# Optimization experiments

Measured on AMD Instinct MI355X. Metric: run time of the kernel, lower is better.

## Reference

```python
import jax, jax.numpy as jnp
import numpy as np

B, S, D, H = 128, 256, 256, 8
EPS = 1e-5

def ln(x, g, b):
    m = x.mean(-1, keepdims=True)
    v = x.var(-1, keepdims=True)
    return (x - m) / jnp.sqrt(v + EPS) * g + b

def setup_inputs() -> dict:
    key = jax.random.key(0)
    ks = jax.random.split(key, 16)
    w = lambda k, sh: (jax.random.normal(k, sh, dtype=jnp.float32) * 0.02)
    HD = H * D
    return {
        "local": jax.random.normal(ks[0], (B, D), dtype=jnp.float32),
        "dist": jax.random.normal(ks[1], (B, S, D), dtype=jnp.float32),
        "sites": jax.random.normal(ks[2], (B, S, D), dtype=jnp.float32),
        "mask": jax.random.randint(ks[3], (B, 1, S), 0, 2).astype(bool),
        "Wq": w(ks[4], (D, HD)), "bq": jnp.zeros((HD,), jnp.float32),
        "gq": jnp.ones((HD,), jnp.float32), "betq": jnp.zeros((HD,), jnp.float32),
        "Wk": w(ks[5], (D, HD)), "bk": jnp.zeros((HD,), jnp.float32),
        "gk": jnp.ones((HD,), jnp.float32), "betk": jnp.zeros((HD,), jnp.float32),
        "Wv": w(ks[6], (D, HD)), "bv": jnp.zeros((HD,), jnp.float32),
        "gv": jnp.ones((HD,), jnp.float32), "betv": jnp.zeros((HD,), jnp.float32),
        "g1": jnp.ones((HD,), jnp.float32), "b1": jnp.zeros((HD,), jnp.float32),
        "Wo": w(ks[7], (HD, D)), "bo": jnp.zeros((D,), jnp.float32),
        "g2": jnp.ones((D,), jnp.float32), "b2": jnp.zeros((D,), jnp.float32),
        "Wa": w(ks[8], (H, 1)), "ba": jnp.zeros((1,), jnp.float32),
        "ga": jnp.ones((1,), jnp.float32), "beta_a": jnp.zeros((1,), jnp.float32),
    }

def reference(local, dist, sites, mask, Wq, bq, gq, betq, Wk, bk, gk, betk,
              Wv, bv, gv, betv, g1, b1, Wo, bo, g2, b2, Wa, ba, ga, beta_a):
    # QKV projections + LayerNorm over H*D
    q = ln(local @ Wq + bq, gq, betq)            # [B, H*D]
    k = ln(dist @ Wk + bk, gk, betk)             # [B, S, H*D]
    v = ln(sites @ Wv + bv, gv, betv)            # [B, S, H*D]
    # split heads, layout [H, B, q/s, D] matching torch permute(2,0,1,3)
    q4 = q.reshape(B, 1, H, D).transpose(2, 0, 1, 3)   # [H,B,1,D]
    k4 = k.reshape(B, S, H, D).transpose(2, 0, 1, 3)   # [H,B,S,D]
    v4 = v.reshape(B, S, H, D).transpose(2, 0, 1, 3)   # [H,B,S,D]
    u = jnp.einsum('hbqd,hbsd->hbqs', q4, k4) / jnp.sqrt(jnp.float32(S))
    u = jnp.where(mask[None], -jnp.inf, u)             # mask [B,1,S] broadcasts over heads
    attn = jax.nn.softmax(u, axis=-1)                  # [H,B,1,S]
    out = jnp.einsum('hbqs,hbsd->hbqd', attn, v4) + q4 # residual add, [H,B,1,D]
    out = out.transpose(1, 2, 0, 3).reshape(B, 1, H * D)
    out = ln(ln(out, g1, b1) @ Wo + bo, g2, b2)        # [B,1,D]
    # faithful raw view: [B,1,H,S] contiguous reinterpreted as [B,S,H]
    attn_r = attn.transpose(1, 2, 0, 3).reshape(B, S, H)
    a = ln(attn_r @ Wa + ba, ga, beta_a)               # [B,S,1]
    a = jnp.swapaxes(a, -1, -2)                        # [B,1,S]
    return (a, out)
```

## Files before the change

### kernel.cpp

```cpp
#include <hip/hip_runtime.h>

#define NB 128
#define NS 256
#define ND 256
#define NH 8
#define NHD 2048
static constexpr float EPS = 1e-5f;

typedef __attribute__((ext_vector_type(8))) short bf8v;
typedef __attribute__((ext_vector_type(4))) float f32x4;

__device__ __forceinline__ short f2bf(float f) {
  unsigned u = __float_as_uint(f);
  unsigned r = (u + 0x7fffu + ((u >> 16) & 1u)) >> 16;
  return (short)r;
}

__device__ __forceinline__ void split8(float4 a, float4 b, bf8v& hi, bf8v& lo) {
  float x[8] = {a.x, a.y, a.z, a.w, b.x, b.y, b.z, b.w};
  bf8v h, l;
#pragma unroll
  for (int i = 0; i < 8; ++i) {
    unsigned u = __float_as_uint(x[i]);
    unsigned hb = (u + 0x7fffu + ((u >> 16) & 1u)) >> 16;
    h[i] = (short)hb;
    float hf = __uint_as_float(hb << 16);
    l[i] = f2bf(x[i] - hf);
  }
  hi = h;
  lo = l;
}

__device__ __forceinline__ float block_reduce_sum(float v, float* red, int t) {
  __syncthreads();
  red[t] = v;
  __syncthreads();
  for (int off = 128; off > 0; off >>= 1) {
    if (t < off) red[t] += red[t + off];
    __syncthreads();
  }
  return red[0];
}

__global__ __launch_bounds__(256) void k_meta(const float* __restrict__ Wk,
                                              const float* __restrict__ bk,
                                              const float* __restrict__ Wv,
                                              const float* __restrict__ bv,
                                              const int* __restrict__ mask_i,
                                              float* __restrict__ kmeta,
                                              float* __restrict__ vmeta,
                                              int* __restrict__ flag) {
  int sel = blockIdx.y, c = blockIdx.x, t = threadIdx.x;
  const float* W = sel ? Wv : Wk;
  const float* bvec = sel ? bv : bk;
  float* meta = sel ? vmeta : kmeta;
  __shared__ float red[256];
  __shared__ int sflag;
  float s_w = 0.f, s_l = 0.f;
  const float* row = W + (size_t)c * NHD;
  for (int j = t; j < NHD; j += 256) { float w = row[j]; s_w += w; s_l += w * bvec[j]; }
  s_w = block_reduce_sum(s_w, red, t);
  s_l = block_reduce_sum(s_l, red, t);
  if (t == 0) { meta[c] = s_w * (1.0f / NHD); meta[256 + c] = s_l * (2.0f / NHD); }
  if (c == 0) {
    float s_b = 0.f, s_b2 = 0.f;
    for (int j = t; j < NHD; j += 256) { float bb = bvec[j]; s_b += bb; s_b2 += bb * bb; }
    s_b = block_reduce_sum(s_b, red, t);
    s_b2 = block_reduce_sum(s_b2, red, t);
    if (t == 0) { meta[512] = s_b * (1.0f / NHD); meta[513] = s_b2 * (1.0f / NHD); }
  }
  if (c == 1 && sel == 0) {
    if (t == 0) sflag = 0;
    __syncthreads();
    int any = 0;
    for (int i = t; i < 8192; i += 256) {
      unsigned v = (unsigned)mask_i[i];
      if (v > 1u) any = 1;
    }
    if (any) atomicOr(&sflag, 1);
    __syncthreads();
    if (t == 0) flag[0] = sflag;
  }
}

__global__ __launch_bounds__(256) void k_aat2(const float* __restrict__ Wk,
                                              const float* __restrict__ Wv,
                                              float* __restrict__ MkP,
                                              float* __restrict__ MvP) {
  int idx = blockIdx.x, bi = 0;
  while (idx >= 8 - bi) { idx -= 8 - bi; ++bi; }
  int bj = bi + idx;
  int sel = blockIdx.y & 1, kchunk = blockIdx.y >> 1;
  const float* A = sel ? Wv : Wk;
  float* outP = (sel ? MvP : MkP) + kchunk * 65536;
  int t = threadIdx.x;
  int w = t >> 6, l = t & 63, r16 = l & 15, ksub = l >> 4;
  __shared__ float red[4][32][33];

  int k0 = kchunk * 512 + w * 128;
  const float* ar0 = A + (size_t)(bi * 32 + r16) * NHD + k0;
  const float* ar1 = ar0 + 16 * NHD;
  const float* br0 = A + (size_t)(bj * 32 + r16) * NHD + k0;
  const float* br1 = br0 + 16 * NHD;

  bf8v ah[2][4], al[2][4], bh[2][4], bl[2][4];
#pragma unroll
  for (int kk = 0; kk < 4; ++kk) {
    int c0 = kk * 32 + ksub * 8;
    split8(*(const float4*)(ar0 + c0), *(const float4*)(ar0 + c0 + 4), ah[0][kk], al[0][kk]);
    split8(*(const float4*)(ar1 + c0), *(const float4*)(ar1 + c0 + 4), ah[1][kk], al[1][kk]);
    split8(*(const float4*)(br0 + c0), *(const float4*)(br0 + c0 + 4), bh[0][kk], bl[0][kk]);
    split8(*(const float4*)(br1 + c0), *(const float4*)(br1 + c0 + 4), bh[1][kk], bl[1][kk]);
  }
  f32x4 acc[2][2];
#pragma unroll
  for (int gi = 0; gi < 2; ++gi)
#pragma unroll
    for (int gj = 0; gj < 2; ++gj) acc[gi][gj] = (f32x4){0.f, 0.f, 0.f, 0.f};
#pragma unroll
  for (int kk = 0; kk < 4; ++kk) {
#pragma unroll
    for (int gi = 0; gi < 2; ++gi)
#pragma unroll
      for (int gj = 0; gj < 2; ++gj) {
        acc[gi][gj] = __builtin_amdgcn_mfma_f32_16x16x32_bf16(ah[gi][kk], bh[gj][kk], acc[gi][gj], 0, 0, 0);
        acc[gi][gj] = __builtin_amdgcn_mfma_f32_16x16x32_bf16(al[gi][kk], bh[gj][kk], acc[gi][gj], 0, 0, 0);
        acc[gi][gj] = __builtin_amdgcn_mfma_f32_16x16x32_bf16(ah[gi][kk], bl[gj][kk], acc[gi][gj], 0, 0, 0);
      }
  }
#pragma unroll
  for (int gi = 0; gi < 2; ++gi)
#pragma unroll
    for (int gj = 0; gj < 2; ++gj)
#pragma unroll
      for (int q = 0; q < 4; ++q)
        red[w][gi * 16 + ksub * 4 + q][gj * 16 + r16] = acc[gi][gj][q];
  __syncthreads();
  int r = t >> 3, c0 = (t & 7) * 4;
#pragma unroll
  for (int c = c0; c < c0 + 4; ++c) {
    float s = (red[0][r][c] + red[1][r][c]) + (red[2][r][c] + red[3][r][c]);
    outP[(size_t)(bi * 32 + r) * 256 + bj * 32 + c] = s;
  }
  if (bi != bj) {
#pragma unroll
    for (int c = c0; c < c0 + 4; ++c) {
      float s = (red[0][c][r] + red[1][c][r]) + (red[2][c][r] + red[3][c][r]);
      outP[(size_t)(bj * 32 + r) * 256 + bi * 32 + c] = s;
    }
  }
}

__global__ __launch_bounds__(256) void k_aat_reduce(const float* __restrict__ MkP,
                                                    const float* __restrict__ MvP,
                                                    short* __restrict__ Mkb,
                                                    short* __restrict__ Mvb) {
  int sel = blockIdx.y;
  const float* P = sel ? MvP : MkP;
  short* O = sel ? Mvb : Mkb;
  int idx = blockIdx.x * 256 + threadIdx.x;
  float s = (P[idx] + P[65536 + idx] + P[131072 + idx] + P[196608 + idx]) * (1.0f / NHD);
  O[idx] = f2bf(s);
}

__global__ __launch_bounds__(256) void k_q1(const float* __restrict__ local,
                                            const float* __restrict__ Wq,
                                            const float* __restrict__ bq,
                                            float* __restrict__ qraw,
                                            float* __restrict__ qpart) {
  int h = blockIdx.x, b = blockIdx.y, t = threadIdx.x;
  __shared__ float ls[256];
  __shared__ float red[256];
  ls[t] = local[b * ND + t];
  __syncthreads();
  int j = h * 256 + t;
  float a0 = 0.f, a1 = 0.f, a2 = 0.f, a3 = 0.f;
  const float* W = Wq + j;
#pragma unroll 4
  for (int c = 0; c < 256; c += 4) {
    a0 = fmaf(ls[c],     W[(size_t)c * NHD], a0);
    a1 = fmaf(ls[c + 1], W[(size_t)(c + 1) * NHD], a1);
    a2 = fmaf(ls[c + 2], W[(size_t)(c + 2) * NHD], a2);
    a3 = fmaf(ls[c + 3], W[(size_t)(c + 3) * NHD], a3);
  }
  float acc = (a0 + a1) + (a2 + a3) + bq[j];
  qraw[(size_t)b * NHD + j] = acc;
  float s1 = block_reduce_sum(acc, red, t);
  float s2 = block_reduce_sum(acc * acc, red, t);
  if (t == 0) { qpart[(b * 8 + h) * 2] = s1; qpart[(b * 8 + h) * 2 + 1] = s2; }
}

__global__ __launch_bounds__(256) void k_wkeff(const float* __restrict__ qraw,
                                               const float* __restrict__ qpart,
                                               const float* __restrict__ gq,
                                               const float* __restrict__ betq,
                                               const float* __restrict__ Wk,
                                               const float* __restrict__ bk,
                                               const float* __restrict__ gk,
                                               const float* __restrict__ betk,
                                               float* __restrict__ wkeff,
                                               float* __restrict__ cbGT) {
  int h = blockIdx.x, b = blockIdx.y, t = threadIdx.x;
  __shared__ float qg[256];
  __shared__ float red[256];
  float s1 = 0.f, s2 = 0.f;
#pragma unroll
  for (int i = 0; i < 8; ++i) { s1 += qpart[(b * 8 + i) * 2]; s2 += qpart[(b * 8 + i) * 2 + 1]; }
  float m = s1 * (1.0f / NHD);
  float var = s2 * (1.0f / NHD) - m * m;
  float is = 1.0f / sqrtf(var + EPS);
  int j = h * 256 + t;
  float q = (qraw[(size_t)b * NHD + j] - m) * is * gq[j] + betq[j];
  float qgv = q * gk[j];
  qg[t] = qgv;
  float cb = block_reduce_sum(bk[j] * qgv, red, t);
  float G = block_reduce_sum(qgv, red, t);
  float T = block_reduce_sum(q * betk[j], red, t);
  float acc = 0.f;
  const float4* wr = (const float4*)(Wk + (size_t)t * NHD + h * 256);
#pragma unroll 4
  for (int d4 = 0; d4 < 64; ++d4) {
    float4 w = wr[d4];
    acc += w.x * qg[d4 * 4] + w.y * qg[d4 * 4 + 1] + w.z * qg[d4 * 4 + 2] + w.w * qg[d4 * 4 + 3];
  }
  wkeff[(size_t)(b * NH + h) * ND + t] = acc;
  if (t == 0) { float* p = cbGT + (b * NH + h) * 4; p[0] = cb; p[1] = G; p[2] = T; }
}

__global__ __launch_bounds__(256) void k_moments(const float* __restrict__ dist,
                                                 const float* __restrict__ sites,
                                                 const short* __restrict__ Mkb,
                                                 const short* __restrict__ Mvb,
                                                 const float* __restrict__ kmeta,
                                                 const float* __restrict__ vmeta,
                                                 float* __restrict__ mk_arr,
                                                 float* __restrict__ sk_arr,
                                                 float* __restrict__ mv_arr,
                                                 float* __restrict__ sv_arr) {
  int sel = blockIdx.y;
  const float* X = sel ? sites : dist;
  const short* Mb = sel ? Mvb : Mkb;
  const float* meta = sel ? vmeta : kmeta;
  float* m_out = sel ? mv_arr : mk_arr;
  float* s_out = sel ? sv_arr : sk_arr;

  int t = threadIdx.x;
  int w = t >> 6;
  int l = t & 63;
  int r16 = l & 15;
  int ksub = l >> 4;
  int srow = t >> 4;
  int scc0 = (t & 15) * 8;

  __shared__ __align__(16) short Tb[4][2][16][40];
  __shared__ __align__(16) short Ms[2][16][264];

  for (int cc = scc0; cc < 32; cc += 128)
    *(bf8v*)&Ms[0][srow][cc] = *(const bf8v*)(Mb + ((size_t)srow << 8) + cc);

  size_t rowA = (size_t)blockIdx.x * 128 + w * 32;
  const float* xr0 = X + (rowA + r16) * 256;
  const float* xr1 = xr0 + 16 * 256;

  bf8v af0[8], af1[8];
  float pm0 = 0.f, pl0 = 0.f, pm1 = 0.f, pl1 = 0.f;
#pragma unroll
  for (int kc = 0; kc < 8; ++kc) {
    int c0 = kc * 32 + ksub * 8;
    float4 wa = *(const float4*)(meta + c0);
    float4 wb = *(const float4*)(meta + c0 + 4);
    float4 la = *(const float4*)(meta + 256 + c0);
    float4 lb = *(const float4*)(meta + 256 + c0 + 4);
    float4 x0a = *(const float4*)(xr0 + c0);
    float4 x0b = *(const float4*)(xr0 + c0 + 4);
    float4 x1a = *(const float4*)(xr1 + c0);
    float4 x1b = *(const float4*)(xr1 + c0 + 4);
    pm0 += x0a.x * wa.x + x0a.y * wa.y + x0a.z * wa.z + x0a.w * wa.w
         + x0b.x * wb.x + x0b.y * wb.y + x0b.z * wb.z + x0b.w * wb.w;
    pl0 += x0a.x * la.x + x0a.y * la.y + x0a.z * la.z + x0a.w * la.w
         + x0b.x * lb.x + x0b.y * lb.y + x0b.z * lb.z + x0b.w * lb.w;
    pm1 += x1a.x * wa.x + x1a.y * wa.y + x1a.z * wa.z + x1a.w * wa.w
         + x1b.x * wb.x + x1b.y * wb.y + x1b.z * wb.z + x1b.w * wb.w;
    pl1 += x1a.x * la.x + x1a.y * la.y + x1a.z * la.z + x1a.w * la.w
         + x1b.x * lb.x + x1b.y * lb.y + x1b.z * lb.z + x1b.w * lb.w;
    bf8v a0, a1;
    a0[0] = f2bf(x0a.x); a0[1] = f2bf(x0a.y); a0[2] = f2bf(x0a.z); a0[3] = f2bf(x0a.w);
    a0[4] = f2bf(x0b.x); a0[5] = f2bf(x0b.y); a0[6] = f2bf(x0b.z); a0[7] = f2bf(x0b.w);
    a1[0] = f2bf(x1a.x); a1[1] = f2bf(x1a.y); a1[2] = f2bf(x1a.z); a1[3] = f2bf(x1a.w);
    a1[4] = f2bf(x1b.x); a1[5] = f2bf(x1b.y); a1[6] = f2bf(x1b.z); a1[7] = f2bf(x1b.w);
    af0[kc] = a0;
    af1[kc] = a1;
  }
  pm0 += __shfl_xor(pm0, 16); pm0 += __shfl_xor(pm0, 32);
  pl0 += __shfl_xor(pl0, 16); pl0 += __shfl_xor(pl0, 32);
  pm1 += __shfl_xor(pm1, 16); pm1 += __shfl_xor(pm1, 32);
  pl1 += __shfl_xor(pl1, 16); pl1 += __shfl_xor(pl1, 32);

  __syncthreads();

  f32x4 y0 = {0.f, 0.f, 0.f, 0.f}, y1 = {0.f, 0.f, 0.f, 0.f};

#pragma unroll
  for (int n = 0; n < 16; ++n) {
    if (n < 15) {
      const int nn = n + 1;
      const int ncols = 32 * ((nn >> 1) + 1);
      for (int cc = scc0; cc < ncols; cc += 128)
        *(bf8v*)&Ms[nn & 1][srow][cc] = *(const bf8v*)(Mb + ((size_t)(nn * 16 + srow) << 8) + cc);
    }
    const int kcd = n >> 1;
    f32x4 ta = {0.f, 0.f, 0.f, 0.f}, tb = {0.f, 0.f, 0.f, 0.f};
#pragma unroll
    for (int kc = 0; kc < kcd; ++kc) {
      bf8v bfv = *(const bf8v*)&Ms[n & 1][r16][kc * 32 + ksub * 8];
      ta = __builtin_amdgcn_mfma_f32_16x16x32_bf16(af0[kc], bfv, ta, 0, 0, 0);
      tb = __builtin_amdgcn_mfma_f32_16x16x32_bf16(af1[kc], bfv, tb, 0, 0, 0);
    }
    ta = ta + ta;
    tb = tb + tb;
    {
      bf8v bfd = *(const bf8v*)&Ms[n & 1][r16][kcd * 32 + ksub * 8];
      ta = __builtin_amdgcn_mfma_f32_16x16x32_bf16(af0[kcd], bfd, ta, 0, 0, 0);
      tb = __builtin_amdgcn_mfma_f32_16x16x32_bf16(af1[kcd], bfd, tb, 0, 0, 0);
    }
#pragma unroll
    for (int q = 0; q < 4; ++q) {
      Tb[w][0][ksub * 4 + q][(n & 1) * 16 + r16] = f2bf(ta[q]);
      Tb[w][1][ksub * 4 + q][(n & 1) * 16 + r16] = f2bf(tb[q]);
    }
    if (n & 1) {
      bf8v a20 = *(const bf8v*)&Tb[w][0][r16][ksub * 8];
      bf8v a21 = *(const bf8v*)&Tb[w][1][r16][ksub * 8];
      y0 = __builtin_amdgcn_mfma_f32_16x16x32_bf16(a20, af0[n >> 1], y0, 0, 0, 0);
      y1 = __builtin_amdgcn_mfma_f32_16x16x32_bf16(a21, af1[n >> 1], y1, 0, 0, 0);
    }
    __syncthreads();
  }

  int qs = r16 & 3;
  float yd0 = (qs == 0) ? y0[0] : (qs == 1) ? y0[1] : (qs == 2) ? y0[2] : y0[3];
  float yd1 = (qs == 0) ? y1[0] : (qs == 1) ? y1[1] : (qs == 2) ? y1[2] : y1[3];
  float bbar = meta[512], cc = meta[513];
  if (ksub == (r16 >> 2)) {
    float m0 = pm0 + bbar;
    float var0 = fmaxf(yd0 + (pl0 + cc) - m0 * m0, 0.0f) + EPS;
    m_out[rowA + r16] = m0;
    s_out[rowA + r16] = 1.0f / sqrtf(var0);
    float m1 = pm1 + bbar;
    float var1 = fmaxf(yd1 + (pl1 + cc) - m1 * m1, 0.0f) + EPS;
    m_out[rowA + 16 + r16] = m1;
    s_out[rowA + 16 + r16] = 1.0f / sqrtf(var1);
  }
}

__global__ __launch_bounds__(512) void k_attn2(const float* __restrict__ dist,
                                               const float* __restrict__ sites,
                                               const int* __restrict__ mask_i,
                                               const int* __restrict__ mflag,
                                               const float* __restrict__ wkeff,
                                               const float* __restrict__ cbGT,
                                               const float* __restrict__ mk_arr,
                                               const float* __restrict__ sk_arr,
                                               const float* __restrict__ mv_arr,
                                               const float* __restrict__ sv_arr,
                                               float* __restrict__ zbuf,
                                               float* __restrict__ bg) {
  int b = blockIdx.x, t = threadIdx.x;
  int w = t >> 6, l = t & 63, r16 = l & 15, ksub = l >> 4;

  __shared__ float us[16][260];
  __shared__ __align__(16) short St[256][72];

  for (int i = t; i < 8 * 260; i += 512) (&us[8][0])[i] = 0.f;

  const int mbytes = mflag[0];

  const float* xr0 = dist + ((size_t)b * NS + w * 32 + r16) * ND;
  const float* xr1 = xr0 + 16 * ND;
  const float* wkp = wkeff + ((size_t)b * NH + (r16 & 7)) * ND;
  f32x4 u0 = {0.f, 0.f, 0.f, 0.f}, u1 = {0.f, 0.f, 0.f, 0.f};
#pragma unroll 2
  for (int kc = 0; kc < 8; ++kc) {
    int c0 = kc * 32 + ksub * 8;
    float4 xa = *(const float4*)(xr0 + c0);
    float4 xb = *(const float4*)(xr0 + c0 + 4);
    float4 ya = *(const float4*)(xr1 + c0);
    float4 yb = *(const float4*)(xr1 + c0 + 4);
    float4 wa = {0.f, 0.f, 0.f, 0.f}, wb = {0.f, 0.f, 0.f, 0.f};
    if (r16 < 8) { wa = *(const float4*)(wkp + c0); wb = *(const float4*)(wkp + c0 + 4); }
    bf8v xh, xl, yh, yl, wh, wl;
    split8(xa, xb, xh, xl);
    split8(ya, yb, yh, yl);
    split8(wa, wb, wh, wl);
    u0 = __builtin_amdgcn_mfma_f32_16x16x32_bf16(xh, wh, u0, 0, 0, 0);
    u0 = __builtin_amdgcn_mfma_f32_16x16x32_bf16(xl, wh, u0, 0, 0, 0);
    u0 = __builtin_amdgcn_mfma_f32_16x16x32_bf16(xh, wl, u0, 0, 0, 0);
    u1 = __builtin_amdgcn_mfma_f32_16x16x32_bf16(yh, wh, u1, 0, 0, 0);
    u1 = __builtin_amdgcn_mfma_f32_16x16x32_bf16(yl, wh, u1, 0, 0, 0);
    u1 = __builtin_amdgcn_mfma_f32_16x16x32_bf16(yh, wl, u1, 0, 0, 0);
  }

  float cb = 0.f, G = 0.f, T = 0.f;
  if (r16 < 8) { const float* p = cbGT + (b * NH + r16) * 4; cb = p[0]; G = p[1]; T = p[2]; }
  const unsigned char* mask_b = (const unsigned char*)mask_i;
#pragma unroll
  for (int g = 0; g < 2; ++g) {
    f32x4 uu = g ? u1 : u0;
    int base = w * 32 + g * 16 + ksub * 4;
    float4 mk4 = *(const float4*)(mk_arr + b * NS + base);
    float4 sk4 = *(const float4*)(sk_arr + b * NS + base);
    int mm[4];
    if (mbytes) {
      mm[0] = mask_b[b * NS + base];     mm[1] = mask_b[b * NS + base + 1];
      mm[2] = mask_b[b * NS + base + 2]; mm[3] = mask_b[b * NS + base + 3];
    } else {
      mm[0] = mask_i[b * NS + base];     mm[1] = mask_i[b * NS + base + 1];
      mm[2] = mask_i[b * NS + base + 2]; mm[3] = mask_i[b * NS + base + 3];
    }
    const float* mkp = (const float*)&mk4;
    const float* skp = (const float*)&sk4;
#pragma unroll
    for (int q = 0; q < 4; ++q) {
      float u = ((uu[q] + cb - mkp[q] * G) * skp[q] + T) * 0.0625f;
      if (mm[q]) u = -1e30f;
      if (r16 < 8) us[r16][base + q] = u;
    }
  }
  __syncthreads();

  {
    int h = w;
    float v[4];
#pragma unroll
    for (int i = 0; i < 4; ++i) v[i] = us[h][l + 64 * i];
    float mx = fmaxf(fmaxf(v[0], v[1]), fmaxf(v[2], v[3]));
    for (int off = 32; off > 0; off >>= 1) mx = fmaxf(mx, __shfl_xor(mx, off));
    float sum = 0.f;
#pragma unroll
    for (int i = 0; i < 4; ++i) { v[i] = expf(v[i] - mx); sum += v[i]; }
    for (int off = 32; off > 0; off >>= 1) sum += __shfl_xor(sum, off);
    float inv = 1.0f / sum;
    float bp = 0.f, gp = 0.f;
#pragma unroll
    for (int i = 0; i < 4; ++i) {
      int s = l + 64 * i;
      float a = v[i] * inv;
      float sv = sv_arr[b * NS + s];
      float mv = mv_arr[b * NS + s];
      float wv = a * sv;
      us[h][s] = wv;
      bp += wv;
      gp += wv * mv;
    }
    for (int off = 32; off > 0; off >>= 1) { bp += __shfl_xor(bp, off); gp += __shfl_xor(gp, off); }
    if (l == 0) { float* p = bg + (b * NH + h) * 2; p[0] = bp; p[1] = gp; }
  }
  __syncthreads();

  f32x4 z0 = {0.f, 0.f, 0.f, 0.f}, z1 = {0.f, 0.f, 0.f, 0.f};
  int half = t >> 8, tc = t & 255;
  for (int chunk = 0; chunk < 4; ++chunk) {
    const float* Sp = sites + ((size_t)b * NS + chunk * 64) * ND + tc;
#pragma unroll
    for (int it = 0; it < 4; ++it) {
      int s8 = (half * 4 + it) * 8;
      bf8v vtmp;
#pragma unroll
      for (int j = 0; j < 8; ++j) vtmp[j] = f2bf(Sp[(size_t)(s8 + j) * ND]);
      *(bf8v*)&St[tc][s8] = vtmp;
    }
    __syncthreads();
#pragma unroll
    for (int kst = 0; kst < 2; ++kst) {
      int sg = chunk * 64 + kst * 32 + ksub * 8;
      int sl0 = kst * 32 + ksub * 8;
      float4 p0 = *(const float4*)&us[r16][sg];
      float4 p1 = *(const float4*)&us[r16][sg + 4];
      bf8v ah, al;
      split8(p0, p1, ah, al);
      bf8v b0 = *(const bf8v*)&St[(2 * w) * 16 + r16][sl0];
      bf8v b1 = *(const bf8v*)&St[(2 * w + 1) * 16 + r16][sl0];
      z0 = __builtin_amdgcn_mfma_f32_16x16x32_bf16(ah, b0, z0, 0, 0, 0);
      z0 = __builtin_amdgcn_mfma_f32_16x16x32_bf16(al, b0, z0, 0, 0, 0);
      z1 = __builtin_amdgcn_mfma_f32_16x16x32_bf16(ah, b1, z1, 0, 0, 0);
      z1 = __builtin_amdgcn_mfma_f32_16x16x32_bf16(al, b1, z1, 0, 0, 0);
    }
    __syncthreads();
  }
  if (ksub < 2) {
#pragma unroll
    for (int q = 0; q < 4; ++q) {
      int h = ksub * 4 + q;
      zbuf[((size_t)b * NH + h) * ND + 2 * w * 16 + r16] = z0[q];
      zbuf[((size_t)b * NH + h) * ND + (2 * w + 1) * 16 + r16] = z1[q];
    }
  }
}

__global__ __launch_bounds__(256) void k_o1(const float* __restrict__ zbuf,
                                            const float* __restrict__ bg,
                                            const float* __restrict__ qraw,
                                            const float* __restrict__ qpart,
                                            const float* __restrict__ gq,
                                            const float* __restrict__ betq,
                                            const float* __restrict__ Wv,
                                            const float* __restrict__ bv,
                                            const float* __restrict__ gv,
                                            const float* __restrict__ betv,
                                            float* __restrict__ o_buf,
                                            float* __restrict__ part1) {
  int h = blockIdx.x, b = blockIdx.y, t = threadIdx.x;
  __shared__ float zs[256];
  __shared__ float red[256];
  zs[t] = zbuf[((size_t)b * NH + h) * ND + t];
  __syncthreads();
  float qs1 = 0.f, qs2 = 0.f;
#pragma unroll
  for (int i = 0; i < 8; ++i) { qs1 += qpart[(b * 8 + i) * 2]; qs2 += qpart[(b * 8 + i) * 2 + 1]; }
  float qm = qs1 * (1.0f / NHD);
  float qvar = qs2 * (1.0f / NHD) - qm * qm;
  float qis = 1.0f / sqrtf(qvar + EPS);
  float bets = bg[(b * NH + h) * 2], gams = bg[(b * NH + h) * 2 + 1];
  int j = h * 256 + t;
  float a0 = 0.f, a1 = 0.f, a2 = 0.f, a3 = 0.f;
  const float* W = Wv + j;
#pragma unroll 4
  for (int c = 0; c < 256; c += 4) {
    a0 = fmaf(zs[c],     W[(size_t)c * NHD], a0);
    a1 = fmaf(zs[c + 1], W[(size_t)(c + 1) * NHD], a1);
    a2 = fmaf(zs[c + 2], W[(size_t)(c + 2) * NHD], a2);
    a3 = fmaf(zs[c + 3], W[(size_t)(c + 3) * NHD], a3);
  }
  float acc = (a0 + a1) + (a2 + a3);
  float qln = (qraw[(size_t)b * NHD + j] - qm) * qis * gq[j] + betq[j];
  float o = gv[j] * (acc + bv[j] * bets - gams) + betv[j] + qln;
  o_buf[(size_t)b * NHD + j] = o;
  float s1 = block_reduce_sum(o, red, t);
  float s2 = block_reduce_sum(o * o, red, t);
  if (t == 0) { part1[(b * 8 + h) * 2] = s1; part1[(b * 8 + h) * 2 + 1] = s2; }
}

__global__ __launch_bounds__(256) void k_o2(const float* __restrict__ o_buf,
                                            const float* __restrict__ part1,
                                            const float* __restrict__ g1,
                                            const float* __restrict__ b1,
                                            const float* __restrict__ Wo,
                                            float* __restrict__ part2) {
  int ks = blockIdx.x, b = blockIdx.y, t = threadIdx.x;
  __shared__ float y1s[256];
  float s1 = 0.f, s2 = 0.f;
#pragma unroll
  for (int i = 0; i < 8; ++i) { s1 += part1[(b * 8 + i) * 2]; s2 += part1[(b * 8 + i) * 2 + 1]; }
  float m = s1 * (1.0f / NHD);
  float var = s2 * (1.0f / NHD) - m * m;
  float is = 1.0f / sqrtf(var + EPS);
  int jj = ks * 256 + t;
  y1s[t] = (o_buf[(size_t)b * NHD + jj] - m) * is * g1[jj] + b1[jj];
  __syncthreads();
  float a0 = 0.f, a1 = 0.f, a2 = 0.f, a3 = 0.f;
  const float* W = Wo + (size_t)ks * 256 * 256 + t;
#pragma unroll 4
  for (int i = 0; i < 256; i += 4) {
    a0 = fmaf(y1s[i],     W[(size_t)i * 256], a0);
    a1 = fmaf(y1s[i + 1], W[(size_t)(i + 1) * 256], a1);
    a2 = fmaf(y1s[i + 2], W[(size_t)(i + 2) * 256], a2);
    a3 = fmaf(y1s[i + 3], W[(size_t)(i + 3) * 256], a3);
  }
  part2[((size_t)ks * NB + b) * 256 + t] = (a0 + a1) + (a2 + a3);
}

__global__ __launch_bounds__(256) void k_o3(const float* __restrict__ part2,
                                            const float* __restrict__ bo,
                                            const float* __restrict__ g2,
                                            const float* __restrict__ b2,
                                            const float* __restrict__ beta_a,
                                            float* __restrict__ out) {
  int b = blockIdx.x, t = threadIdx.x;
  __shared__ float red[256];
  float acc = bo[t];
#pragma unroll
  for (int ks = 0; ks < 8; ++ks) acc += part2[((size_t)ks * NB + b) * 256 + t];
  float q1 = block_reduce_sum(acc, red, t);
  float q2 = block_reduce_sum(acc * acc, red, t);
  float m2 = q1 * (1.0f / 256.0f);
  float v2 = q2 * (1.0f / 256.0f) - m2 * m2;
  float is2 = 1.0f / sqrtf(v2 + EPS);
  out[NB * NS + b * 256 + t] = (acc - m2) * is2 * g2[t] + b2[t];
  out[b * 256 + t] = beta_a[0];
}

extern "C" void kernel_launch(void* const* d_in, const int* in_sizes, int n_in,
                              void* d_out, int out_size, void* d_ws, size_t ws_size,
                              hipStream_t stream) {
  (void)in_sizes; (void)n_in; (void)out_size; (void)ws_size;
  const float* local = (const float*)d_in[0];
  const float* dist  = (const float*)d_in[1];
  const float* sites = (const float*)d_in[2];
  const int*   mask  = (const int*)d_in[3];
  const float* Wq   = (const float*)d_in[4];
  const float* bq   = (const float*)d_in[5];
  const float* gq   = (const float*)d_in[6];
  const float* betq = (const float*)d_in[7];
  const float* Wk   = (const float*)d_in[8];
  const float* bk   = (const float*)d_in[9];
  const float* gk   = (const float*)d_in[10];
  const float* betk = (const float*)d_in[11];
  const float* Wv   = (const float*)d_in[12];
  const float* bv   = (const float*)d_in[13];
  const float* gv   = (const float*)d_in[14];
  const float* betv = (const float*)d_in[15];
  const float* g1   = (const float*)d_in[16];
  const float* b1   = (const float*)d_in[17];
  const float* Wo   = (const float*)d_in[18];
  const float* bo   = (const float*)d_in[19];
  const float* g2   = (const float*)d_in[20];
  const float* b2   = (const float*)d_in[21];
  const float* beta_a = (const float*)d_in[25];
  float* out = (float*)d_out;

  float* ws = (float*)d_ws;
  float* MkP   = ws;
  float* MvP   = MkP + 262144;
  short* Mkb   = (short*)(MvP + 262144);
  short* Mvb   = Mkb + 65536;
  float* kmeta = (float*)(Mvb + 65536);
  float* vmeta = kmeta + 1024;
  float* qraw  = vmeta + 1024;
  float* wkeff = qraw + 262144;
  float* cbGT  = wkeff + 262144;
  float* mk_arr = cbGT + 4096;
  float* sk_arr = mk_arr + 32768;
  float* mv_arr = sk_arr + 32768;
  float* sv_arr = mv_arr + 32768;
  float* zbuf  = sv_arr + 32768;
  float* bg    = zbuf + 262144;
  int*   mflag = (int*)(bg + 2048);
  float* part1 = (float*)(mflag + 16);
  float* qpart = part1 + 2048;

  float* o_buf = qraw;
  float* part2 = MvP;

  k_meta<<<dim3(256, 2), dim3(256), 0, stream>>>(Wk, bk, Wv, bv, mask, kmeta, vmeta, mflag);
  k_aat2<<<dim3(36, 8), dim3(256), 0, stream>>>(Wk, Wv, MkP, MvP);
  k_aat_reduce<<<dim3(256, 2), dim3(256), 0, stream>>>(MkP, MvP, Mkb, Mvb);
  k_q1<<<dim3(8, 128), dim3(256), 0, stream>>>(local, Wq, bq, qraw, qpart);
  k_wkeff<<<dim3(8, 128), dim3(256), 0, stream>>>(qraw, qpart, gq, betq, Wk, bk, gk, betk,
                                                  wkeff, cbGT);
  k_moments<<<dim3(256, 2), dim3(256), 0, stream>>>(dist, sites, Mkb, Mvb, kmeta, vmeta,
                                                    mk_arr, sk_arr, mv_arr, sv_arr);
  k_attn2<<<dim3(128), dim3(512), 0, stream>>>(dist, sites, mask, mflag, wkeff, cbGT,
                                               mk_arr, sk_arr, mv_arr, sv_arr, zbuf, bg);
  k_o1<<<dim3(8, 128), dim3(256), 0, stream>>>(zbuf, bg, qraw, qpart, gq, betq,
                                               Wv, bv, gv, betv, o_buf, part1);
  k_o2<<<dim3(8, 128), dim3(256), 0, stream>>>(o_buf, part1, g1, b1, Wo, part2);
  k_o3<<<dim3(128), dim3(256), 0, stream>>>(part2, bo, g2, b2, beta_a, out);
}
```

Before: 141.8 us.

## Compute LN variance quadratic form without LDS staging, using global loads and shuffles

The per-row quadratic form x^T M x is computed as before with MFMA on the upper-triangle tiles of M. M fragments are now read straight from global memory instead of being staged through double-buffered LDS, which removes the per-iteration __syncthreads. The second MFMA (T·x) is replaced by elementwise FMAs against fp32 x values reloaded from global memory, followed by a 16-lane shuffle reduction. This trades barriers and LDS traffic for more global/L2 loads and scalar FMAs, and the second product now uses fp32 x instead of bf16.

```diff
diff --git a/kernel.cpp b/kernel.cpp
--- a/kernel.cpp
+++ b/kernel.cpp
@@ -249,14 +249,6 @@
   int l = t & 63;
   int r16 = l & 15;
   int ksub = l >> 4;
-  int srow = t >> 4;
-  int scc0 = (t & 15) * 8;
-
-  __shared__ __align__(16) short Tb[4][2][16][40];
-  __shared__ __align__(16) short Ms[2][16][264];
-
-  for (int cc = scc0; cc < 32; cc += 128)
-    *(bf8v*)&Ms[0][srow][cc] = *(const bf8v*)(Mb + ((size_t)srow << 8) + cc);
 
   size_t rowA = (size_t)blockIdx.x * 128 + w * 32;
   const float* xr0 = X + (rowA + r16) * 256;
@@ -296,50 +288,48 @@
   pm1 += __shfl_xor(pm1, 16); pm1 += __shfl_xor(pm1, 32);
   pl1 += __shfl_xor(pl1, 16); pl1 += __shfl_xor(pl1, 32);
 
-  __syncthreads();
-
-  f32x4 y0 = {0.f, 0.f, 0.f, 0.f}, y1 = {0.f, 0.f, 0.f, 0.f};
+  f32x4 yv0 = {0.f, 0.f, 0.f, 0.f}, yv1 = {0.f, 0.f, 0.f, 0.f};
+  const float* xb0 = X + rowA * 256;
+  const float* xb1 = X + (rowA + 16) * 256;
 
 #pragma unroll
   for (int n = 0; n < 16; ++n) {
-    if (n < 15) {
-      const int nn = n + 1;
-      const int ncols = 32 * ((nn >> 1) + 1);
-      for (int cc = scc0; cc < ncols; cc += 128)
-        *(bf8v*)&Ms[nn & 1][srow][cc] = *(const bf8v*)(Mb + ((size_t)(nn * 16 + srow) << 8) + cc);
-    }
     const int kcd = n >> 1;
     f32x4 ta = {0.f, 0.f, 0.f, 0.f}, tb = {0.f, 0.f, 0.f, 0.f};
 #pragma unroll
     for (int kc = 0; kc < kcd; ++kc) {
-      bf8v bfv = *(const bf8v*)&Ms[n & 1][r16][kc * 32 + ksub * 8];
+      bf8v bfv = *(const bf8v*)(Mb + ((size_t)(n * 16 + r16) << 8) + kc * 32 + ksub * 8);
       ta = __builtin_amdgcn_mfma_f32_16x16x32_bf16(af0[kc], bfv, ta, 0, 0, 0);
       tb = __builtin_amdgcn_mfma_f32_16x16x32_bf16(af1[kc], bfv, tb, 0, 0, 0);
     }
     ta = ta + ta;
     tb = tb + tb;
     {
-      bf8v bfd = *(const bf8v*)&Ms[n & 1][r16][kcd * 32 + ksub * 8];
+      bf8v bfd = *(const bf8v*)(Mb + ((size_t)(n * 16 + r16) << 8) + kcd * 32 + ksub * 8);
       ta = __builtin_amdgcn_mfma_f32_16x16x32_bf16(af0[kcd], bfd, ta, 0, 0, 0);
       tb = __builtin_amdgcn_mfma_f32_16x16x32_bf16(af1[kcd], bfd, tb, 0, 0, 0);
     }
 #pragma unroll
     for (int q = 0; q < 4; ++q) {
-      Tb[w][0][ksub * 4 + q][(n & 1) * 16 + r16] = f2bf(ta[q]);
-      Tb[w][1][ksub * 4 + q][(n & 1) * 16 + r16] = f2bf(tb[q]);
-    }
-    if (n & 1) {
-      bf8v a20 = *(const bf8v*)&Tb[w][0][r16][ksub * 8];
-      bf8v a21 = *(const bf8v*)&Tb[w][1][r16][ksub * 8];
-      y0 = __builtin_amdgcn_mfma_f32_16x16x32_bf16(a20, af0[n >> 1], y0, 0, 0, 0);
-      y1 = __builtin_amdgcn_mfma_f32_16x16x32_bf16(a21, af1[n >> 1], y1, 0, 0, 0);
-    }
-    __syncthreads();
+      float xv0 = xb0[(size_t)(ksub * 4 + q) * 256 + n * 16 + r16];
+      float xv1 = xb1[(size_t)(ksub * 4 + q) * 256 + n * 16 + r16];
+      yv0[q] = fmaf(ta[q], xv0, yv0[q]);
+      yv1[q] = fmaf(tb[q], xv1, yv1[q]);
+    }
+  }
+
+#pragma unroll
+  for (int off = 1; off < 16; off <<= 1) {
+#pragma unroll
+    for (int q = 0; q < 4; ++q) {
+      yv0[q] += __shfl_xor(yv0[q], off);
+      yv1[q] += __shfl_xor(yv1[q], off);
+    }
   }
 
   int qs = r16 & 3;
-  float yd0 = (qs == 0) ? y0[0] : (qs == 1) ? y0[1] : (qs == 2) ? y0[2] : y0[3];
-  float yd1 = (qs == 0) ? y1[0] : (qs == 1) ? y1[1] : (qs == 2) ? y1[2] : y1[3];
+  float yd0 = (qs == 0) ? yv0[0] : (qs == 1) ? yv0[1] : (qs == 2) ? yv0[2] : yv0[3];
+  float yd1 = (qs == 0) ? yv1[0] : (qs == 1) ? yv1[1] : (qs == 2) ? yv1[2] : yv1[3];
   float bbar = meta[512], cc = meta[513];
   if (ksub == (r16 >> 2)) {
     float m0 = pm0 + bbar;
```

New measurement: 151.0 us. 6.5% more time.
